# Kernel optimization log

Hardware: AMD Instinct MI355X
Metric: run time of the kernel (lower is better)

The kernel has to match this reference:

```python
import jax, jax.numpy as jnp
import numpy as np

L, B, H, IN = 4, 256, 1024, 1024

def setup_inputs() -> dict:
    key = jax.random.key(0)
    ks = jax.random.split(key, 7)
    return {
        "x": jax.random.normal(ks[0], (B, IN), jnp.float32),
        "h0": jax.random.normal(ks[1], (L, B, H), jnp.float32),
        "c0": jax.random.normal(ks[2], (L, B, H), jnp.float32),
        "w_ih": jax.random.normal(ks[3], (L, 4 * H, IN), jnp.float32) * 0.02,
        "w_hh": jax.random.normal(ks[4], (L, 4 * H, H), jnp.float32) * 0.02,
        "b_ih": jax.random.normal(ks[5], (L, 4 * H), jnp.float32) * 0.02,
        "b_hh": jax.random.normal(ks[6], (L, 4 * H), jnp.float32) * 0.02,
    }

def _lstm_cell(inp, h, c, wi, wh, bi, bh):
    # gates: (B, 4H), PyTorch gate order i, f, g, o
    gates = jnp.dot(inp, wi.T) + jnp.dot(h, wh.T) + bi + bh
    i_g, f_g, g_g, o_g = jnp.split(gates, 4, axis=-1)
    c_new = jax.nn.sigmoid(f_g) * c + jax.nn.sigmoid(i_g) * jnp.tanh(g_g)
    h_new = jax.nn.sigmoid(o_g) * jnp.tanh(c_new)
    return h_new, c_new

def reference(x, h0, c0, w_ih, w_hh, b_ih, b_hh):
    # Sequential over layers (inter-layer dependency); dropout is identity (eval mode / p=0).
    inp = x
    hs, cs = [], []
    for i in range(h0.shape[0]):
        h, c = _lstm_cell(inp, h0[i], c0[i], w_ih[i], w_hh[i], b_ih[i], b_hh[i])
        hs.append(h)
        cs.append(c)
        inp = h
    return jnp.stack(hs, axis=0), jnp.stack(cs, axis=0)
```

## Files before the change

### kernel.cpp

```cpp
#include <hip/hip_runtime.h>

#define NLAYER 4
#define BATCH  256
#define HID    1024

typedef float f32x4 __attribute__((ext_vector_type(4)));
typedef short short8 __attribute__((ext_vector_type(8)));

#define BARRIER() __asm__ __volatile__("s_waitcnt lgkmcnt(0)\ns_barrier" ::: "memory")

__device__ __forceinline__ unsigned short f2bf(float f) {
  unsigned int u = __float_as_uint(f);
  unsigned int r = u + 0x7fffu + ((u >> 16) & 1u);
  return (unsigned short)(r >> 16);
}
__device__ __forceinline__ float sigm(float x) { return 1.f / (1.f + __expf(-x)); }
__device__ __forceinline__ float tanh_(float x) { return 2.f / (1.f + __expf(-2.f * x)) - 1.f; }

__device__ __forceinline__ int lds_w(int r, int kk0) {
  return r * 64 + (((kk0 >> 3) ^ (r & 7)) << 3) + (kk0 & 7);
}
__device__ __forceinline__ int lds_r(int row, int c) {
  return row * 64 + ((c ^ (row & 7)) << 3);
}

__global__ __launch_bounds__(512, 2) void lstm_fused(
    const float* __restrict__ A0, const float* __restrict__ A1,
    const float* __restrict__ W0, const float* __restrict__ W1,
    const float* __restrict__ bi, const float* __restrict__ bh,
    const float* __restrict__ c0l,
    float* __restrict__ hout, float* __restrict__ cout) {
  __shared__ union U {
    unsigned short stage[2][2][64 * 64];
    float sg[4 * 64 * 17];
  } sm;
  __shared__ float bsum[64];

  const int tid  = threadIdx.x;
  const int h0c  = blockIdx.x * 16;
  const int m0   = blockIdx.y * 64;
  const int lane = tid & 63;
  const int w    = tid >> 6;
  const int wm   = w & 3;
  const int wcol = w >> 2;
  const int lrow = lane & 15, lq = lane >> 4;

  if (tid < 64) {
    int g = tid >> 4, hc = tid & 15;
    bsum[tid] = bi[g * 1024 + h0c + hc] + bh[g * 1024 + h0c + hc];
  }

  const int r0  = tid >> 4;
  const int kk0 = (tid & 15) << 2;
  const int wr0 = (r0 >> 4) * 1024 + h0c + (r0 & 15);

  const float* pA0 = A0 + (size_t)(m0 + r0) * 1024 + kk0;
  const float* pA1 = A1 + (size_t)(m0 + r0) * 1024 + kk0;
  const float* pW0 = W0 + (size_t)wr0 * 1024 + kk0;
  const float* pW1 = W1 + (size_t)wr0 * 1024 + kk0;

  const int erow = tid >> 3;
  const int ehp  = (tid & 7) * 2;
  float2 cp = *reinterpret_cast<const float2*>(
      c0l + (size_t)(m0 + erow) * 1024 + h0c + ehp);

  float4 ra[4][2], rb[4][2];
  auto loadAB = [&](int kt, int s) {
    const float* pa = (kt < 16 ? pA0 : pA1) + (kt & 15) * 64;
    const float* pb = (kt < 16 ? pW0 : pW1) + (kt & 15) * 64;
    ra[s][0] = *reinterpret_cast<const float4*>(pa);
    ra[s][1] = *reinterpret_cast<const float4*>(pa + 32 * 1024);
    rb[s][0] = *reinterpret_cast<const float4*>(pb);
    rb[s][1] = *reinterpret_cast<const float4*>(pb + 2048 * 1024);
  };

  f32x4 acc[2];
  acc[0] = (f32x4){0.f, 0.f, 0.f, 0.f};
  acc[1] = (f32x4){0.f, 0.f, 0.f, 0.f};

  loadAB(0, 0); loadAB(1, 1); loadAB(2, 2);

  for (int kt4 = 0; kt4 < 32; kt4 += 4) {
#pragma unroll
    for (int ks = 0; ks < 4; ++ks) {
      const int kt  = kt4 + ks;
      const int buf = ks & 1;
#pragma unroll
      for (int i = 0; i < 2; ++i) {
        int r = r0 + (i << 5);
        ushort4 pa, pb;
        pa.x = f2bf(ra[ks][i].x); pa.y = f2bf(ra[ks][i].y);
        pa.z = f2bf(ra[ks][i].z); pa.w = f2bf(ra[ks][i].w);
        pb.x = f2bf(rb[ks][i].x); pb.y = f2bf(rb[ks][i].y);
        pb.z = f2bf(rb[ks][i].z); pb.w = f2bf(rb[ks][i].w);
        *reinterpret_cast<ushort4*>(&sm.stage[buf][0][lds_w(r, kk0)]) = pa;
        *reinterpret_cast<ushort4*>(&sm.stage[buf][1][lds_w(r, kk0)]) = pb;
      }
      if (kt < 29) loadAB(kt + 3, (ks + 3) & 3);
      BARRIER();
#pragma unroll
      for (int kk = 0; kk < 64; kk += 32) {
        const int cb = kk >> 3;
        short8 af = *reinterpret_cast<const short8*>(
            &sm.stage[buf][0][lds_r(wm * 16 + lrow, cb + lq)]);
        short8 bf0 = *reinterpret_cast<const short8*>(
            &sm.stage[buf][1][lds_r(wcol * 32 + lrow, cb + lq)]);
        short8 bf1 = *reinterpret_cast<const short8*>(
            &sm.stage[buf][1][lds_r(wcol * 32 + 16 + lrow, cb + lq)]);
        acc[0] = __builtin_amdgcn_mfma_f32_16x16x32_bf16(af, bf0, acc[0], 0, 0, 0);
        acc[1] = __builtin_amdgcn_mfma_f32_16x16x32_bf16(af, bf1, acc[1], 0, 0, 0);
      }
    }
  }

  BARRIER();

#pragma unroll
  for (int nt = 0; nt < 2; ++nt) {
    int gate = wcol * 2 + nt;
    int rowb = wm * 16 + lq * 4;
#pragma unroll
    for (int r = 0; r < 4; ++r)
      sm.sg[gate * 1088 + (rowb + r) * 17 + lrow] = acc[nt][r];
  }
  BARRIER();

  {
    float cpa[2] = {cp.x, cp.y};
    float hva[2], cva[2];
#pragma unroll
    for (int e = 0; e < 2; ++e) {
      int hc = ehp + e;
      float gi = sm.sg[0 * 1088 + erow * 17 + hc] + bsum[0  + hc];
      float gf = sm.sg[1 * 1088 + erow * 17 + hc] + bsum[16 + hc];
      float gg = sm.sg[2 * 1088 + erow * 17 + hc] + bsum[32 + hc];
      float go = sm.sg[3 * 1088 + erow * 17 + hc] + bsum[48 + hc];
      float cn = sigm(gf) * cpa[e] + sigm(gi) * tanh_(gg);
      cva[e] = cn;
      hva[e] = sigm(go) * tanh_(cn);
    }
    float2 hv; hv.x = hva[0]; hv.y = hva[1];
    float2 cv; cv.x = cva[0]; cv.y = cva[1];
    *reinterpret_cast<float2*>(hout + (size_t)(m0 + erow) * 1024 + h0c + ehp) = hv;
    *reinterpret_cast<float2*>(cout + (size_t)(m0 + erow) * 1024 + h0c + ehp) = cv;
  }
}

extern "C" void kernel_launch(void* const* d_in, const int* in_sizes, int n_in,
                              void* d_out, int out_size, void* d_ws, size_t ws_size,
                              hipStream_t stream) {
  const float* x    = (const float*)d_in[0];
  const float* h0   = (const float*)d_in[1];
  const float* c0   = (const float*)d_in[2];
  const float* w_ih = (const float*)d_in[3];
  const float* w_hh = (const float*)d_in[4];
  const float* b_ih = (const float*)d_in[5];
  const float* b_hh = (const float*)d_in[6];
  float* out = (float*)d_out;

  const size_t BH = (size_t)BATCH * HID;
  const size_t WL = (size_t)4 * HID * HID;

  for (int l = 0; l < NLAYER; ++l) {
    const float* A0 = (l == 0) ? x : out + (size_t)(l - 1) * BH;
    lstm_fused<<<dim3(64, 4), 512, 0, stream>>>(
        A0, h0 + (size_t)l * BH,
        w_ih + (size_t)l * WL, w_hh + (size_t)l * WL,
        b_ih + (size_t)l * 4096, b_hh + (size_t)l * 4096,
        c0 + (size_t)l * BH,
        out + (size_t)l * BH, out + (size_t)NLAYER * BH + (size_t)l * BH);
  }
}
```

Measured before the change: 263.6 us.

## Pre-pack operands to swizzled bf16 and stream them via global-to-LDS DMA

Adds two pre-pass kernels that convert weights, x and h0 to bf16 in a tile-swizzled layout inside the workspace. Each layer kernel then streams its A and B tiles straight into a 4-stage LDS ring with global_load_lds, replacing the register round-trip and in-loop bf16 conversion. Each layer's epilogue also writes its h output in packed bf16 form as the next layer's A operand. This takes conversion work and register pressure off the GEMM loop and deepens the prefetch. In exchange, the weight pack runs on every call and adds extra fp32 read and bf16 write traffic.

```diff
diff --git a/kernel.cpp b/kernel.cpp
--- a/kernel.cpp
+++ b/kernel.cpp
@@ -6,8 +6,14 @@
 
 typedef float f32x4 __attribute__((ext_vector_type(4)));
 typedef short short8 __attribute__((ext_vector_type(8)));
-
-#define BARRIER() __asm__ __volatile__("s_waitcnt lgkmcnt(0)\ns_barrier" ::: "memory")
+typedef unsigned short ushort_t;
+
+#define BAR()     asm volatile("s_barrier")
+#define WAITV(n)  asm volatile("s_waitcnt vmcnt(" #n ")")
+#define DSR(d, a) asm volatile("ds_read_b128 %0, %1" : "=v"(d) : "v"(a))
+#define LGKM0_TIE6(a,b,c,d,e,f) \
+  asm volatile("s_waitcnt lgkmcnt(0)" : "+v"(a),"+v"(b),"+v"(c),"+v"(d),"+v"(e),"+v"(f))
+#define FULLBAR() asm volatile("s_waitcnt lgkmcnt(0)\ns_barrier" ::: "memory")
 
 __device__ __forceinline__ unsigned short f2bf(float f) {
   unsigned int u = __float_as_uint(f);
@@ -17,113 +23,152 @@
 __device__ __forceinline__ float sigm(float x) { return 1.f / (1.f + __expf(-x)); }
 __device__ __forceinline__ float tanh_(float x) { return 2.f / (1.f + __expf(-2.f * x)) - 1.f; }
 
-__device__ __forceinline__ int lds_w(int r, int kk0) {
-  return r * 64 + (((kk0 >> 3) ^ (r & 7)) << 3) + (kk0 & 7);
-}
-__device__ __forceinline__ int lds_r(int row, int c) {
-  return row * 64 + ((c ^ (row & 7)) << 3);
-}
-
-__global__ __launch_bounds__(512, 2) void lstm_fused(
-    const float* __restrict__ A0, const float* __restrict__ A1,
-    const float* __restrict__ W0, const float* __restrict__ W1,
+__device__ __forceinline__ void dma16(const void* g, void* l) {
+  __builtin_amdgcn_global_load_lds(
+      (const __attribute__((address_space(1))) unsigned int*)g,
+      (__attribute__((address_space(3))) unsigned int*)l, 16, 0, 0);
+}
+
+
+__global__ __launch_bounds__(256) void pack_w(const float* __restrict__ w_ih,
+                                              const float* __restrict__ w_hh,
+                                              ushort_t* __restrict__ wpk) {
+  int tid = blockIdx.x * 256 + threadIdx.x;
+  int lane = tid & 63;
+  int kt   = (tid >> 9) & 31;
+  int nb   = (tid >> 14) & 63;
+  int l    = tid >> 20;
+  int g    = (tid >> 6) & 7;
+  int r = g * 8 + (lane >> 3);
+  int c = (lane & 7) ^ (lane >> 3);
+  int wrow = (r >> 4) * 1024 + nb * 16 + (r & 15);
+  const float* src = (kt < 16 ? w_ih : w_hh) + (size_t)l * 4194304
+                   + (size_t)wrow * 1024 + (kt & 15) * 64 + c * 8;
+  float4 a = *(const float4*)src, b = *(const float4*)(src + 4);
+  short8 pk;
+  pk[0] = (short)f2bf(a.x); pk[1] = (short)f2bf(a.y);
+  pk[2] = (short)f2bf(a.z); pk[3] = (short)f2bf(a.w);
+  pk[4] = (short)f2bf(b.x); pk[5] = (short)f2bf(b.y);
+  pk[6] = (short)f2bf(b.z); pk[7] = (short)f2bf(b.w);
+  *(short8*)(wpk + (size_t)tid * 8) = pk;
+}
+
+__global__ __launch_bounds__(256) void pack_a(const float* __restrict__ x,
+                                              const float* __restrict__ h0,
+                                              ushort_t* __restrict__ apk) {
+  int t = blockIdx.x * 256 + threadIdx.x;
+  int lane = t & 63;
+  int r8 = lane >> 3;
+  int c = (lane & 7) ^ r8;
+  const float* src;
+  ushort_t* dst;
+  if (t < 32768) {
+    int g = (t >> 6) & 7, kt = (t >> 9) & 15, mb = t >> 13;
+    int m = mb * 64 + g * 8 + r8;
+    src = x + (size_t)m * 1024 + kt * 64 + c * 8;
+    dst = apk + (size_t)mb * 131072 + (size_t)kt * 4096 + g * 512 + lane * 8;
+  } else {
+    int u = t - 32768;
+    int g = (u >> 6) & 7, kt16 = (u >> 9) & 15, mb = (u >> 13) & 3, l = u >> 15;
+    int m = mb * 64 + g * 8 + r8;
+    src = h0 + (size_t)l * 262144 + (size_t)m * 1024 + kt16 * 64 + c * 8;
+    dst = apk + (size_t)l * 524288 + (size_t)mb * 131072
+        + (size_t)(16 + kt16) * 4096 + g * 512 + lane * 8;
+  }
+  float4 a = *(const float4*)src, b = *(const float4*)(src + 4);
+  short8 pk;
+  pk[0] = (short)f2bf(a.x); pk[1] = (short)f2bf(a.y);
+  pk[2] = (short)f2bf(a.z); pk[3] = (short)f2bf(a.w);
+  pk[4] = (short)f2bf(b.x); pk[5] = (short)f2bf(b.y);
+  pk[6] = (short)f2bf(b.z); pk[7] = (short)f2bf(b.w);
+  *(short8*)dst = pk;
+}
+
+__global__ __launch_bounds__(512) void lstm_fused(
+    const ushort_t* __restrict__ apk, const ushort_t* __restrict__ wpk,
     const float* __restrict__ bi, const float* __restrict__ bh,
     const float* __restrict__ c0l,
-    float* __restrict__ hout, float* __restrict__ cout) {
+    float* __restrict__ hout, float* __restrict__ cout,
+    ushort_t* __restrict__ apk_next) {
   __shared__ union U {
-    unsigned short stage[2][2][64 * 64];
+    ushort_t stage[4][2][4096];
     float sg[4 * 64 * 17];
   } sm;
   __shared__ float bsum[64];
 
-  const int tid  = threadIdx.x;
-  const int h0c  = blockIdx.x * 16;
-  const int m0   = blockIdx.y * 64;
+  const int tid = threadIdx.x;
+  const int nb = blockIdx.x;
+  const int mb = blockIdx.y;
+  const int h0c = nb * 16;
+  const int m0 = mb * 64;
   const int lane = tid & 63;
-  const int w    = tid >> 6;
-  const int wm   = w & 3;
-  const int wcol = w >> 2;
+  const int w = tid >> 6;
+  const int wm = w & 3, wcol = w >> 2;
   const int lrow = lane & 15, lq = lane >> 4;
 
   if (tid < 64) {
     int g = tid >> 4, hc = tid & 15;
     bsum[tid] = bi[g * 1024 + h0c + hc] + bh[g * 1024 + h0c + hc];
   }
-
-  const int r0  = tid >> 4;
-  const int kk0 = (tid & 15) << 2;
-  const int wr0 = (r0 >> 4) * 1024 + h0c + (r0 & 15);
-
-  const float* pA0 = A0 + (size_t)(m0 + r0) * 1024 + kk0;
-  const float* pA1 = A1 + (size_t)(m0 + r0) * 1024 + kk0;
-  const float* pW0 = W0 + (size_t)wr0 * 1024 + kk0;
-  const float* pW1 = W1 + (size_t)wr0 * 1024 + kk0;
-
-  const int erow = tid >> 3;
-  const int ehp  = (tid & 7) * 2;
-  float2 cp = *reinterpret_cast<const float2*>(
-      c0l + (size_t)(m0 + erow) * 1024 + h0c + ehp);
-
-  float4 ra[4][2], rb[4][2];
-  auto loadAB = [&](int kt, int s) {
-    const float* pa = (kt < 16 ? pA0 : pA1) + (kt & 15) * 64;
-    const float* pb = (kt < 16 ? pW0 : pW1) + (kt & 15) * 64;
-    ra[s][0] = *reinterpret_cast<const float4*>(pa);
-    ra[s][1] = *reinterpret_cast<const float4*>(pa + 32 * 1024);
-    rb[s][0] = *reinterpret_cast<const float4*>(pb);
-    rb[s][1] = *reinterpret_cast<const float4*>(pb + 2048 * 1024);
-  };
-
-  f32x4 acc[2];
-  acc[0] = (f32x4){0.f, 0.f, 0.f, 0.f};
-  acc[1] = (f32x4){0.f, 0.f, 0.f, 0.f};
-
-  loadAB(0, 0); loadAB(1, 1); loadAB(2, 2);
-
-  for (int kt4 = 0; kt4 < 32; kt4 += 4) {
-#pragma unroll
-    for (int ks = 0; ks < 4; ++ks) {
-      const int kt  = kt4 + ks;
-      const int buf = ks & 1;
-#pragma unroll
-      for (int i = 0; i < 2; ++i) {
-        int r = r0 + (i << 5);
-        ushort4 pa, pb;
-        pa.x = f2bf(ra[ks][i].x); pa.y = f2bf(ra[ks][i].y);
-        pa.z = f2bf(ra[ks][i].z); pa.w = f2bf(ra[ks][i].w);
-        pb.x = f2bf(rb[ks][i].x); pb.y = f2bf(rb[ks][i].y);
-        pb.z = f2bf(rb[ks][i].z); pb.w = f2bf(rb[ks][i].w);
-        *reinterpret_cast<ushort4*>(&sm.stage[buf][0][lds_w(r, kk0)]) = pa;
-        *reinterpret_cast<ushort4*>(&sm.stage[buf][1][lds_w(r, kk0)]) = pb;
-      }
-      if (kt < 29) loadAB(kt + 3, (ks + 3) & 3);
-      BARRIER();
-#pragma unroll
-      for (int kk = 0; kk < 64; kk += 32) {
-        const int cb = kk >> 3;
-        short8 af = *reinterpret_cast<const short8*>(
-            &sm.stage[buf][0][lds_r(wm * 16 + lrow, cb + lq)]);
-        short8 bf0 = *reinterpret_cast<const short8*>(
-            &sm.stage[buf][1][lds_r(wcol * 32 + lrow, cb + lq)]);
-        short8 bf1 = *reinterpret_cast<const short8*>(
-            &sm.stage[buf][1][lds_r(wcol * 32 + 16 + lrow, cb + lq)]);
-        acc[0] = __builtin_amdgcn_mfma_f32_16x16x32_bf16(af, bf0, acc[0], 0, 0, 0);
-        acc[1] = __builtin_amdgcn_mfma_f32_16x16x32_bf16(af, bf1, acc[1], 0, 0, 0);
-      }
+  const int erow = tid >> 3, ehp = (tid & 7) * 2;
+  float2 cp = *(const float2*)(c0l + (size_t)(m0 + erow) * 1024 + h0c + ehp);
+
+  const char* srcA = (const char*)(apk + (size_t)mb * 131072 + w * 512 + lane * 8);
+  const char* srcB = (const char*)(wpk + (size_t)nb * 131072 + w * 512 + lane * 8);
+
+  unsigned smb = (unsigned)(uintptr_t)(__attribute__((address_space(3))) void*)&sm;
+  const int rA = wm * 16 + lrow;
+  const int rB0 = wcol * 32 + lrow, rB1 = rB0 + 16;
+#define SWZ(r, c) (((r) >> 3) * 64 + ((r) & 7) * 8 + (((c) ^ (r)) & 7))
+  unsigned oA0 = smb + SWZ(rA, lq) * 16,         oA1 = smb + SWZ(rA, 4 + lq) * 16;
+  unsigned oB00 = smb + 8192 + SWZ(rB0, lq) * 16, oB01 = smb + 8192 + SWZ(rB0, 4 + lq) * 16;
+  unsigned oB10 = smb + 8192 + SWZ(rB1, lq) * 16, oB11 = smb + 8192 + SWZ(rB1, 4 + lq) * 16;
+#undef SWZ
+
+  f32x4 acc0 = {0.f, 0.f, 0.f, 0.f}, acc1 = {0.f, 0.f, 0.f, 0.f};
+
+#pragma unroll
+  for (int t = 0; t < 3; ++t) {
+    dma16(srcA, &sm.stage[t][0][w * 512]);
+    dma16(srcB, &sm.stage[t][1][w * 512]);
+    srcA += 8192; srcB += 8192;
+  }
+  WAITV(4);
+
+  for (int kt = 0; kt < 32; ++kt) {
+    BAR();
+    if (kt <= 28) {
+      int b3 = (kt + 3) & 3;
+      dma16(srcA, &sm.stage[b3][0][w * 512]);
+      dma16(srcB, &sm.stage[b3][1][w * 512]);
+      srcA += 8192; srcB += 8192;
     }
-  }
-
-  BARRIER();
+    unsigned boff = (unsigned)(kt & 3) * 16384u;
+    short8 af0, af1, b00, b01, b10, b11;
+    DSR(af0, oA0 + boff); DSR(b00, oB00 + boff); DSR(b10, oB10 + boff);
+    DSR(af1, oA1 + boff); DSR(b01, oB01 + boff); DSR(b11, oB11 + boff);
+    LGKM0_TIE6(af0, af1, b00, b01, b10, b11);
+    acc0 = __builtin_amdgcn_mfma_f32_16x16x32_bf16(af0, b00, acc0, 0, 0, 0);
+    acc1 = __builtin_amdgcn_mfma_f32_16x16x32_bf16(af0, b10, acc1, 0, 0, 0);
+    acc0 = __builtin_amdgcn_mfma_f32_16x16x32_bf16(af1, b01, acc0, 0, 0, 0);
+    acc1 = __builtin_amdgcn_mfma_f32_16x16x32_bf16(af1, b11, acc1, 0, 0, 0);
+    if (kt <= 28)      { WAITV(4); }
+    else if (kt == 29) { WAITV(2); }
+    else if (kt == 30) { WAITV(0); }
+  }
+
+  FULLBAR();
 
 #pragma unroll
   for (int nt = 0; nt < 2; ++nt) {
     int gate = wcol * 2 + nt;
     int rowb = wm * 16 + lq * 4;
+    const f32x4& a = nt ? acc1 : acc0;
 #pragma unroll
     for (int r = 0; r < 4; ++r)
-      sm.sg[gate * 1088 + (rowb + r) * 17 + lrow] = acc[nt][r];
-  }
-  BARRIER();
+      sm.sg[gate * 1088 + (rowb + r) * 17 + lrow] = a[r];
+  }
+  FULLBAR();
 
   {
     float cpa[2] = {cp.x, cp.y};
@@ -141,8 +186,19 @@
     }
     float2 hv; hv.x = hva[0]; hv.y = hva[1];
     float2 cv; cv.x = cva[0]; cv.y = cva[1];
-    *reinterpret_cast<float2*>(hout + (size_t)(m0 + erow) * 1024 + h0c + ehp) = hv;
-    *reinterpret_cast<float2*>(cout + (size_t)(m0 + erow) * 1024 + h0c + ehp) = cv;
+    *(float2*)(hout + (size_t)(m0 + erow) * 1024 + h0c + ehp) = hv;
+    *(float2*)(cout + (size_t)(m0 + erow) * 1024 + h0c + ehp) = cv;
+    if (apk_next) {
+      int g = erow >> 3;
+#pragma unroll
+      for (int e = 0; e < 2; ++e) {
+        int k = h0c + ehp + e;
+        int cc = (k >> 3) & 7, j = k & 7;
+        int i = (erow & 7) * 8 + ((cc ^ erow) & 7);
+        apk_next[(size_t)mb * 131072 + (size_t)(k >> 6) * 4096 + g * 512 + i * 8 + j] =
+            f2bf(hva[e]);
+      }
+    }
   }
 }
 
@@ -158,16 +214,19 @@
   const float* b_hh = (const float*)d_in[6];
   float* out = (float*)d_out;
 
+  ushort_t* Wpk = (ushort_t*)d_ws;
+  ushort_t* Apk = Wpk + (size_t)4 * 8388608;
+
+  pack_w<<<16384, 256, 0, stream>>>(w_ih, w_hh, Wpk);
+  pack_a<<<640, 256, 0, stream>>>(x, h0, Apk);
+
   const size_t BH = (size_t)BATCH * HID;
-  const size_t WL = (size_t)4 * HID * HID;
-
   for (int l = 0; l < NLAYER; ++l) {
-    const float* A0 = (l == 0) ? x : out + (size_t)(l - 1) * BH;
     lstm_fused<<<dim3(64, 4), 512, 0, stream>>>(
-        A0, h0 + (size_t)l * BH,
-        w_ih + (size_t)l * WL, w_hh + (size_t)l * WL,
+        Apk + (size_t)l * 524288, Wpk + (size_t)l * 8388608,
         b_ih + (size_t)l * 4096, b_hh + (size_t)l * 4096,
         c0 + (size_t)l * BH,
-        out + (size_t)l * BH, out + (size_t)NLAYER * BH + (size_t)l * BH);
-  }
-}
+        out + (size_t)l * BH, out + (size_t)NLAYER * BH + (size_t)l * BH,
+        (l < NLAYER - 1) ? Apk + (size_t)(l + 1) * 524288 : (ushort_t*)nullptr);
+  }
+}
```

After: 224.6 us. -14.8%, faster.
